# Kernel optimization log

Hardware: AMD Instinct MI355X
Metric: run time of the kernel (lower is better)

## Reference

```python
import jax, jax.numpy as jnp
import numpy as np

N_NODES = 50000
N_EDGES = 1600000
NUM_BASIS = 10
HIDDEN = 64
MAX_RADIUS = 3.0
WEIGHT_NUMEL = 5  # paths: (0x0->0),(0x1->1),(1x0->1),(1x1->0),(1x1->1)


def setup_inputs() -> dict:
    key = jax.random.key(0)
    k1, k2, k3, k4, k5 = jax.random.split(key, 5)
    f_1 = jax.random.normal(k1, (N_NODES, 4), dtype=jnp.float32)
    pos = jax.random.uniform(k2, (N_NODES, 3), dtype=jnp.float32) * MAX_RADIUS
    edge_index = jax.random.randint(k3, (2, N_EDGES), 0, N_NODES, dtype=jnp.int64)
    # radial MLP params (e3nn FullyConnectedNet init: std-normal weights)
    W1 = jax.random.normal(k4, (NUM_BASIS, HIDDEN), dtype=jnp.float32)
    W2 = jax.random.normal(k5, (HIDDEN, WEIGHT_NUMEL), dtype=jnp.float32)
    return {"f_1": f_1, "pos": pos, "W1": W1, "W2": W2, "edge_index": edge_index}


def _forward(f_1, pos, W1, W2, edge_index):
    row, col = edge_index[0], edge_index[1]
    num_nodes = f_1.shape[0]
    num_neighbors = edge_index.shape[1] / num_nodes

    edge_vec = pos[row] - pos[col]                      # [E,3]
    r2 = jnp.sum(edge_vec * edge_vec, axis=-1)
    r = jnp.sqrt(jnp.maximum(r2, 1e-12))                # [E]
    unit = edge_vec / r[:, None]

    # spherical harmonics 0e+1e, component normalization, e3nn (y,z,x) order
    sh = jnp.concatenate(
        [jnp.ones_like(unit[:, :1]), jnp.sqrt(3.0) * unit[:, [1, 2, 0]]], axis=-1
    )                                                   # [E,4]

    # soft_one_hot_linspace, basis='smooth_finite', cutoff=True
    values = jnp.linspace(0.0, MAX_RADIUS, NUM_BASIS + 2)[1:-1]
    step = values[1] - values[0]
    diff = (r[:, None] - values) / step                 # [E,num_basis]
    inside = jnp.abs(diff) < 1.0
    d = jnp.where(inside, diff, 0.0)
    C = 1.14136 * float(np.e) ** 2
    emb = jnp.where(inside, C * jnp.exp(-1.0 / (1.0 + d) - 1.0 / (1.0 - d)), 0.0)

    # e3nn FullyConnectedNet [num_basis, hidden, weight_numel] with relu
    # hidden: act normalized to unit 2nd moment (relu -> *sqrt(2)); weights /sqrt(fan_in)
    h = jax.nn.relu(emb @ (W1 / jnp.sqrt(float(NUM_BASIS)))) * jnp.sqrt(2.0)
    w = h @ (W2 / jnp.sqrt(float(HIDDEN)))              # [E,5]

    # FullyConnectedTensorProduct (0e+1e) x (0e+1e) -> (0e+1e), per-edge weights
    x = f_1[row]
    x0, xv = x[:, 0], x[:, 1:4]
    y0, yv = sh[:, 0], sh[:, 1:4]
    inv_s3 = 1.0 / jnp.sqrt(3.0)
    inv_s6 = 1.0 / jnp.sqrt(6.0)
    # output 0e: fan-in 2 paths -> norm sqrt(1/2)
    out0 = jnp.sqrt(0.5) * (
        w[:, 0] * x0 * y0 + w[:, 3] * jnp.sum(xv * yv, axis=-1) * inv_s3
    )
    # output 1e: fan-in 3 paths -> norm sqrt(3/3)=1
    outv = (
        w[:, 1:2] * x0[:, None] * yv * inv_s3
        + w[:, 2:3] * xv * y0[:, None] * inv_s3
        + w[:, 4:5] * jnp.cross(xv, yv) * inv_s6
    )
    f_edge = jnp.concatenate([out0[:, None], outv], axis=-1)  # [E,4]

    out = jax.ops.segment_sum(f_edge, col, num_segments=num_nodes)
    return out / jnp.sqrt(num_neighbors).astype(out.dtype)


def reference(f_1, pos, W1, W2, edge_index):
    return _forward(f_1, pos, W1, W2, edge_index)
```

## Files before the change

### kernel.cpp

```cpp
#include <hip/hip_runtime.h>
#include <math.h>

#define N_NODES_C 50000
#define N_EDGES_C 1600000
#define EPB 1024
#define NBLK_E 1563
#define NBLK_N 196
#define TBL 256

#define NREG 25
#define RSH 11
#define RNODES 2048
#define CAPL 17
#define NCHG 32

#define QSCALE 1024.0f
#define QINV   (1.0f / 1024.0f)

__device__ __forceinline__ int detect_is64_block(const void* eidx, int t, int* lds_flag) {
    if (t < 64) {
        const long long* p = (const long long*)eidx;
        bool ok = true;
        for (int k = 0; k < 4; ++k) {
            long long v = p[t * 4 + k];
            ok &= (v >= 0 && v < (long long)N_NODES_C);
        }
        unsigned long long m = __ballot(ok);
        if (t == 0) *lds_flag = (m == ~0ull) ? 1 : 0;
    }
    __syncthreads();
    return *lds_flag;
}

__device__ __forceinline__ int load_col(const void* eidx, int is64, int e) {
    return is64 ? (int)((const long long*)eidx)[N_EDGES_C + e]
                : ((const int*)eidx)[N_EDGES_C + e];
}
__device__ __forceinline__ int load_row(const void* eidx, int is64, int e) {
    return is64 ? (int)((const long long*)eidx)[e]
                : ((const int*)eidx)[e];
}

__device__ __forceinline__ void edge_quant(const float* __restrict__ f1,
                                           const float* __restrict__ pos,
                                           const float* __restrict__ w1s,
                                           const float* __restrict__ W2,
                                           int row, int col, int v[4]) {
    v[0] = v[1] = v[2] = v[3] = 0;
    float px = pos[row * 3 + 0] - pos[col * 3 + 0];
    float py = pos[row * 3 + 1] - pos[col * 3 + 1];
    float pz = pos[row * 3 + 2] - pos[col * 3 + 2];
    float r2 = px * px + py * py + pz * pz;
    float r = sqrtf(fmaxf(r2, 1e-12f));
    float inv_r = 1.0f / r;
    float ux = px * inv_r, uy = py * inv_r, uz = pz * inv_r;
    const float SQ3 = 1.7320508075688772f;
    float yv0 = SQ3 * uy, yv1 = SQ3 * uz, yv2 = SQ3 * ux;

    const float C = 8.433573069075486f;
    float tt = r * (11.0f / 3.0f);
    int k1 = (int)tt;
    float d = tt - (float)k1;
    float e0 = 0.f, e1 = 0.f;
    int b0 = 0, b1 = 0;
    if (k1 >= 1 && k1 <= 10) {
        b0 = k1 - 1;
        e0 = C * __expf(-1.0f / (1.0f + d) - 1.0f / (1.0f - d));
    }
    int k2 = k1 + 1;
    if (k2 <= 10 && d > 0.f) {
        b1 = k2 - 1;
        float d2 = d - 1.0f;
        e1 = C * __expf(-1.0f / (1.0f + d2) - 1.0f / (1.0f - d2));
    }
    if (e0 == 0.f && e1 == 0.f) return;

    const float* r0 = &w1s[b0 * 68];
    const float* r1 = &w1s[b1 * 68];
    float w0 = 0.f, w1a = 0.f, w2a = 0.f, w3 = 0.f, w4 = 0.f;
#pragma unroll
    for (int j = 0; j < 64; j += 4) {
        float4 a = *(const float4*)(r0 + j);
        float4 b = *(const float4*)(r1 + j);
        float h0 = fmaxf(e0 * a.x + e1 * b.x, 0.f);
        float h1 = fmaxf(e0 * a.y + e1 * b.y, 0.f);
        float h2 = fmaxf(e0 * a.z + e1 * b.z, 0.f);
        float h3 = fmaxf(e0 * a.w + e1 * b.w, 0.f);
        w0  += h0 * W2[(j + 0) * 5 + 0] + h1 * W2[(j + 1) * 5 + 0] + h2 * W2[(j + 2) * 5 + 0] + h3 * W2[(j + 3) * 5 + 0];
        w1a += h0 * W2[(j + 0) * 5 + 1] + h1 * W2[(j + 1) * 5 + 1] + h2 * W2[(j + 2) * 5 + 1] + h3 * W2[(j + 3) * 5 + 1];
        w2a += h0 * W2[(j + 0) * 5 + 2] + h1 * W2[(j + 1) * 5 + 2] + h2 * W2[(j + 2) * 5 + 2] + h3 * W2[(j + 3) * 5 + 2];
        w3  += h0 * W2[(j + 0) * 5 + 3] + h1 * W2[(j + 1) * 5 + 3] + h2 * W2[(j + 2) * 5 + 3] + h3 * W2[(j + 3) * 5 + 3];
        w4  += h0 * W2[(j + 0) * 5 + 4] + h1 * W2[(j + 1) * 5 + 4] + h2 * W2[(j + 2) * 5 + 4] + h3 * W2[(j + 3) * 5 + 4];
    }
    const float SC = 0.05590169943749474f;
    w0 *= SC; w1a *= SC; w2a *= SC; w3 *= SC; w4 *= SC;

    float4 x = *(const float4*)(f1 + row * 4);
    float x0 = x.x, xv0 = x.y, xv1 = x.z, xv2 = x.w;

    const float INV_S3 = 0.5773502691896258f;
    const float INV_S6 = 0.4082482904638631f;
    const float SQH    = 0.7071067811865476f;
    const float INV_SQRT_NN = 0.17677669529663687f;

    float dotxy = xv0 * yv0 + xv1 * yv1 + xv2 * yv2;
    float out0 = SQH * (w0 * x0 + w3 * dotxy * INV_S3) * INV_SQRT_NN;
    float cx0 = xv1 * yv2 - xv2 * yv1;
    float cx1 = xv2 * yv0 - xv0 * yv2;
    float cx2 = xv0 * yv1 - xv1 * yv0;
    float o1 = (w1a * x0 * yv0 * INV_S3 + w2a * xv0 * INV_S3 + w4 * cx0 * INV_S6) * INV_SQRT_NN;
    float o2 = (w1a * x0 * yv1 * INV_S3 + w2a * xv1 * INV_S3 + w4 * cx1 * INV_S6) * INV_SQRT_NN;
    float o3 = (w1a * x0 * yv2 * INV_S3 + w2a * xv2 * INV_S3 + w4 * cx2 * INV_S6) * INV_SQRT_NN;

    v[0] = min(8191, max(-8191, (int)rintf(out0 * QSCALE)));
    v[1] = min(8191, max(-8191, (int)rintf(o1   * QSCALE)));
    v[2] = min(8191, max(-8191, (int)rintf(o2   * QSCALE)));
    v[3] = min(8191, max(-8191, (int)rintf(o3   * QSCALE)));
}

__device__ __forceinline__ unsigned long long edge_q(
        float prx, float pry, float prz, float4 xx,
        float pcx, float pcy, float pcz,
        const float* tC0, const float* tC1, const float* tC2,
        const float* tC3, const float* tC4) {
    float px = prx - pcx;
    float py = pry - pcy;
    float pz = prz - pcz;
    float r2 = px * px + py * py + pz * pz;
    float r = sqrtf(fmaxf(r2, 1e-12f));
    float inv_r = 1.0f / r;
    float uv0 = py * inv_r, uv1 = pz * inv_r, uv2 = px * inv_r;

    float ft = fminf(r * (255.0f / 3.0f), 255.0f);
    int idx = min((int)ft, TBL - 2);
    float fr = ft - (float)idx;
    float c0 = fmaf(fr, tC0[idx + 1] - tC0[idx], tC0[idx]);
    float c1 = fmaf(fr, tC1[idx + 1] - tC1[idx], tC1[idx]);
    float c2 = fmaf(fr, tC2[idx + 1] - tC2[idx], tC2[idx]);
    float c3 = fmaf(fr, tC3[idx + 1] - tC3[idx], tC3[idx]);
    float c4 = fmaf(fr, tC4[idx + 1] - tC4[idx], tC4[idx]);

    float x0 = xx.x, xv0 = xx.y, xv1 = xx.z, xv2 = xx.w;

    float dotxy = xv0 * uv0 + xv1 * uv1 + xv2 * uv2;
    float out0 = c0 * x0 + c3 * dotxy;
    float cx0 = xv1 * uv2 - xv2 * uv1;
    float cx1 = xv2 * uv0 - xv0 * uv2;
    float cx2 = xv0 * uv1 - xv1 * uv0;
    float c1x = c1 * x0;
    float o1 = c1x * uv0 + c2 * xv0 + c4 * cx0;
    float o2 = c1x * uv1 + c2 * xv1 + c4 * cx1;
    float o3 = c1x * uv2 + c2 * xv2 + c4 * cx2;

    int v0 = min(8191, max(-8191, (int)rintf(out0 * QSCALE)));
    int v1 = min(8191, max(-8191, (int)rintf(o1 * QSCALE)));
    int v2 = min(8191, max(-8191, (int)rintf(o2 * QSCALE)));
    int v3 = min(8191, max(-8191, (int)rintf(o3 * QSCALE)));

    return (unsigned long long)((long long)v0 + ((long long)v1 << 16)
         + ((long long)v2 << 32) + ((long long)v3 << 48));
}

__global__ __launch_bounds__(256)
void binscatter_kernel(const float* __restrict__ f1, const float* __restrict__ pos,
                       const float* __restrict__ W1, const float* __restrict__ W2,
                       const void* __restrict__ eidx,
                       unsigned* __restrict__ gOff,
                       unsigned* __restrict__ rcG,
                       float* __restrict__ nodeq,
                       float* __restrict__ tG) {
    __shared__ unsigned rcbuf[EPB];
    __shared__ unsigned stageRc[EPB];
    __shared__ unsigned histS[32];
    __shared__ unsigned gBaseS[32];
    __shared__ unsigned localBaseS[32];
    __shared__ unsigned cursorLocS[32];
    __shared__ int flag_s;
    const int t = threadIdx.x;
    float* w1s = (float*)stageRc;
    if (blockIdx.x == 0) {
        for (int i = t; i < 640; i += 256) w1s[(i >> 6) * 68 + (i & 63)] = W1[i];
    }
    if (t < 32) histS[t] = 0u;
    const int is64 = detect_is64_block(eidx, t, &flag_s);

    if (blockIdx.x == 0) {
        float tt = (float)t * (11.0f / 255.0f);
        int k1 = (int)tt;
        float d = tt - (float)k1;
        const float C = 8.433573069075486f;
        float e0 = 0.f, e1 = 0.f;
        int b0 = 0, b1 = 0;
        if (k1 >= 1 && k1 <= 10) {
            b0 = k1 - 1;
            e0 = C * __expf(-1.0f / (1.0f + d) - 1.0f / (1.0f - d));
        }
        int k2 = k1 + 1;
        if (k2 <= 10 && d > 0.f) {
            b1 = k2 - 1;
            float d2 = d - 1.0f;
            e1 = C * __expf(-1.0f / (1.0f + d2) - 1.0f / (1.0f - d2));
        }
        float w0 = 0.f, w1 = 0.f, w2 = 0.f, w3 = 0.f, w4 = 0.f;
        const float* r0 = &w1s[b0 * 68];
        const float* r1 = &w1s[b1 * 68];
#pragma unroll
        for (int j = 0; j < 64; j += 4) {
            float4 a = *(const float4*)(r0 + j);
            float4 b = *(const float4*)(r1 + j);
            float h0 = fmaxf(e0 * a.x + e1 * b.x, 0.f);
            float h1 = fmaxf(e0 * a.y + e1 * b.y, 0.f);
            float h2 = fmaxf(e0 * a.z + e1 * b.z, 0.f);
            float h3 = fmaxf(e0 * a.w + e1 * b.w, 0.f);
            w0 += h0 * W2[(j + 0) * 5 + 0] + h1 * W2[(j + 1) * 5 + 0] + h2 * W2[(j + 2) * 5 + 0] + h3 * W2[(j + 3) * 5 + 0];
            w1 += h0 * W2[(j + 0) * 5 + 1] + h1 * W2[(j + 1) * 5 + 1] + h2 * W2[(j + 2) * 5 + 1] + h3 * W2[(j + 3) * 5 + 1];
            w2 += h0 * W2[(j + 0) * 5 + 2] + h1 * W2[(j + 1) * 5 + 2] + h2 * W2[(j + 2) * 5 + 2] + h3 * W2[(j + 3) * 5 + 2];
            w3 += h0 * W2[(j + 0) * 5 + 3] + h1 * W2[(j + 1) * 5 + 3] + h2 * W2[(j + 2) * 5 + 3] + h3 * W2[(j + 3) * 5 + 3];
            w4 += h0 * W2[(j + 0) * 5 + 4] + h1 * W2[(j + 1) * 5 + 4] + h2 * W2[(j + 2) * 5 + 4] + h3 * W2[(j + 3) * 5 + 4];
        }
        const float SC  = 0.05590169943749474f;
        const float ISN = 0.17677669529663687f;
        const float SQH = 0.7071067811865476f;
        const float INV_S3 = 0.5773502691896258f;
        const float INV_S6 = 0.4082482904638631f;
        const float SQ3 = 1.7320508075688772f;
        float base = SC * ISN;
        tG[0 * TBL + t] = SQH * base * w0;
        tG[1 * TBL + t] = base * w1;
        tG[2 * TBL + t] = INV_S3 * base * w2;
        tG[3 * TBL + t] = SQH * base * w3;
        tG[4 * TBL + t] = INV_S6 * SQ3 * base * w4;
    }

    const int e0b = blockIdx.x * EPB;
    const int nedge = min(EPB, N_EDGES_C - e0b);
    for (int i = t; i < nedge; i += 256) {
        int row = load_row(eidx, is64, e0b + i);
        int col = load_col(eidx, is64, e0b + i);
        rcbuf[i] = ((unsigned)row << 16) | (unsigned)col;
        atomicAdd(&histS[col >> RSH], 1u);
    }
    {
        int n = blockIdx.x * 256 + t;
        if (blockIdx.x < NBLK_N && n < N_NODES_C) {
            float4 f = *(const float4*)(f1 + 4 * n);
            float4 p;
            p.x = pos[3 * n + 0];
            p.y = pos[3 * n + 1];
            p.z = pos[3 * n + 2];
            p.w = 0.f;
            *(float4*)(nodeq + 8 * n)     = p;
            *(float4*)(nodeq + 8 * n + 4) = f;
        }
    }
    __syncthreads();
    if (t == 0) {
        unsigned run = 0u;
        for (int b = 0; b < 32; ++b) {
            localBaseS[b] = run;
            cursorLocS[b] = run;
            run += histS[b];
        }
    }
    if (t < 32) {
        gBaseS[t] = ((unsigned)t << CAPL) + atomicAdd(&gOff[t], histS[t]);
    }
    __syncthreads();
    for (int i = t; i < nedge; i += 256) {
        unsigned rc = rcbuf[i];
        int b = (int)((rc & 0xFFFFu) >> RSH);
        unsigned p = atomicAdd(&cursorLocS[b], 1u);
        stageRc[p] = rc;
    }
    __syncthreads();
    for (int i = t; i < nedge; i += 256) {
        unsigned rc = stageRc[i];
        int b = (int)((rc & 0xFFFFu) >> RSH);
        unsigned dst = gBaseS[b] + ((unsigned)i - localBaseS[b]);
        unsigned lim = ((unsigned)(b + 1)) << CAPL;
        if (dst < lim) rcG[dst] = rc;
    }
}

__global__ __launch_bounds__(512)
void mgather_kernel(const unsigned* __restrict__ rcG,
                    const unsigned* __restrict__ gOff,
                    const float* __restrict__ pos,
                    const float* __restrict__ nodeq,
                    const float* __restrict__ tG,
                    unsigned long long* __restrict__ partials) {
    __shared__ unsigned long long accs[RNODES];
    __shared__ float posx[RNODES];
    __shared__ float posy[RNODES];
    __shared__ float posz[RNODES];
    __shared__ float tC0[TBL];
    __shared__ float tC1[TBL];
    __shared__ float tC2[TBL];
    __shared__ float tC3[TBL];
    __shared__ float tC4[TBL];
    const int t = threadIdx.x;
    const int B = blockIdx.x;
    const int c = blockIdx.y;
    if (t < TBL) {
        tC0[t] = tG[0 * TBL + t];
        tC1[t] = tG[1 * TBL + t];
        tC2[t] = tG[2 * TBL + t];
        tC3[t] = tG[3 * TBL + t];
        tC4[t] = tG[4 * TBL + t];
    }
    const int nb0 = B << RSH;
    for (int j = t; j < RNODES; j += 512) {
        accs[j] = 0ull;
        int n = nb0 + j;
        if (n < N_NODES_C) {
            posx[j] = pos[3 * n + 0];
            posy[j] = pos[3 * n + 1];
            posz[j] = pos[3 * n + 2];
        }
    }
    __syncthreads();

    unsigned cnt = min(gOff[B], (unsigned)(1u << CAPL));
    unsigned i0 = (unsigned)(((unsigned long long)cnt * (unsigned)c) / NCHG);
    unsigned i1 = (unsigned)(((unsigned long long)cnt * (unsigned)(c + 1)) / NCHG);
    const unsigned* src = rcG + ((size_t)B << CAPL);

    unsigned i = i0 + t;
    for (; i + 512 < i1; i += 1024) {
        unsigned rcA = src[i];
        unsigned rcB = src[i + 512];
        int rowA = (int)(rcA >> 16), lcA = (int)(rcA & (RNODES - 1));
        int rowB = (int)(rcB >> 16), lcB = (int)(rcB & (RNODES - 1));
        const float4* nrA = (const float4*)(nodeq + ((size_t)rowA << 3));
        const float4* nrB = (const float4*)(nodeq + ((size_t)rowB << 3));
        float4 prA = nrA[0];
        float4 xxA = nrA[1];
        float4 prB = nrB[0];
        float4 xxB = nrB[1];
        float pcxA = posx[lcA], pcyA = posy[lcA], pczA = posz[lcA];
        float pcxB = posx[lcB], pcyB = posy[lcB], pczB = posz[lcB];
        unsigned long long QA = edge_q(prA.x, prA.y, prA.z, xxA, pcxA, pcyA, pczA,
                                       tC0, tC1, tC2, tC3, tC4);
        unsigned long long QB = edge_q(prB.x, prB.y, prB.z, xxB, pcxB, pcyB, pczB,
                                       tC0, tC1, tC2, tC3, tC4);
        atomicAdd(&accs[lcA], QA);
        atomicAdd(&accs[lcB], QB);
    }
    for (; i < i1; i += 512) {
        unsigned rc = src[i];
        int row = (int)(rc >> 16), lc = (int)(rc & (RNODES - 1));
        const float4* nr = (const float4*)(nodeq + ((size_t)row << 3));
        float4 pr = nr[0];
        float4 xx = nr[1];
        unsigned long long Q = edge_q(pr.x, pr.y, pr.z, xx, posx[lc], posy[lc], posz[lc],
                                      tC0, tC1, tC2, tC3, tC4);
        atomicAdd(&accs[lc], Q);
    }
    __syncthreads();
    unsigned long long* dst = partials + (((size_t)(B * NCHG + c)) << RSH);
    for (int j = t; j < RNODES; j += 512) dst[j] = accs[j];
}

__global__ __launch_bounds__(256)
void reduce6_kernel(const unsigned long long* __restrict__ partials, float* __restrict__ out) {
    int n = blockIdx.x * 256 + threadIdx.x;
    if (n >= N_NODES_C) return;
    int B = n >> RSH;
    int lc = n & (RNODES - 1);
    const unsigned long long* src = partials + (((size_t)(B * NCHG)) << RSH) + lc;
    unsigned long long s = 0ull;
#pragma unroll
    for (int c = 0; c < NCHG; ++c) s += src[(size_t)c << RSH];
    long long T = (long long)s;
    int s0 = (int)(short)(T & 0xFFFF); T = (T - s0) >> 16;
    int s1 = (int)(short)(T & 0xFFFF); T = (T - s1) >> 16;
    int s2 = (int)(short)(T & 0xFFFF); T = (T - s2) >> 16;
    int s3 = (int)T;
    float4 o;
    o.x = (float)s0 * QINV;
    o.y = (float)s1 * QINV;
    o.z = (float)s2 * QINV;
    o.w = (float)s3 * QINV;
    *(float4*)(out + 4 * n) = o;
}

__global__ __launch_bounds__(256)
void init_acc(unsigned long long* __restrict__ acc,
              const void* __restrict__ eidx, int* __restrict__ flag) {
    int i = blockIdx.x * 256 + threadIdx.x;
    if (i < N_NODES_C) acc[i] = 0ull;
    if (blockIdx.x == 0 && threadIdx.x < 64) {
        const long long* p = (const long long*)eidx;
        bool ok = true;
        for (int k = 0; k < 4; ++k) {
            long long v = p[threadIdx.x * 4 + k];
            ok &= (v >= 0 && v < (long long)N_NODES_C);
        }
        unsigned long long m = __ballot(ok);
        if (threadIdx.x == 0) *flag = (m == ~0ull) ? 1 : 0;
    }
}

__global__ __launch_bounds__(256)
void reduce_unpack(const unsigned long long* __restrict__ acc, float* __restrict__ out) {
    int n = blockIdx.x * 256 + threadIdx.x;
    if (n >= N_NODES_C) return;
    long long T = (long long)acc[n];
    int s0 = (int)(short)(T & 0xFFFF); T = (T - s0) >> 16;
    int s1 = (int)(short)(T & 0xFFFF); T = (T - s1) >> 16;
    int s2 = (int)(short)(T & 0xFFFF); T = (T - s2) >> 16;
    int s3 = (int)T;
    float4 o;
    o.x = (float)s0 * QINV; o.y = (float)s1 * QINV;
    o.z = (float)s2 * QINV; o.w = (float)s3 * QINV;
    *(float4*)(out + 4 * n) = o;
}

__global__ __launch_bounds__(256)
void equi_conv_atomic(const float* __restrict__ f1, const float* __restrict__ pos,
                      const float* __restrict__ W1, const float* __restrict__ W2,
                      const void* __restrict__ eidx, const int* __restrict__ flag_p,
                      unsigned long long* __restrict__ acc) {
    __shared__ float w1s[10 * 68];
    const int tid = threadIdx.x;
    for (int i = tid; i < 640; i += 256) w1s[(i >> 6) * 68 + (i & 63)] = W1[i];
    __syncthreads();
    const int e = blockIdx.x * 256 + tid;
    if (e >= N_EDGES_C) return;
    const int is64 = *flag_p;
    int row = load_row(eidx, is64, e);
    int col = load_col(eidx, is64, e);
    int v[4];
    edge_quant(f1, pos, w1s, W2, row, col, v);
    if (v[0] | v[1] | v[2] | v[3]) {
        unsigned long long P = (unsigned long long)((long long)v[0] + ((long long)v[1] << 16)
                             + ((long long)v[2] << 32) + ((long long)v[3] << 48));
        __hip_atomic_fetch_add(acc + col, P, __ATOMIC_RELAXED, __HIP_MEMORY_SCOPE_AGENT);
    }
}

extern "C" void kernel_launch(void* const* d_in, const int* in_sizes, int n_in,
                              void* d_out, int out_size, void* d_ws, size_t ws_size,
                              hipStream_t stream) {
    const float* f1  = (const float*)d_in[0];
    const float* pos = (const float*)d_in[1];
    const float* W1  = (const float*)d_in[2];
    const float* W2  = (const float*)d_in[3];
    const void*  eix = d_in[4];
    float* out = (float*)d_out;

    const size_t offRC = 0;
    const size_t szRC  = ((size_t)32 << CAPL) * 4;
    const size_t offC  = offRC + szRC;
    const size_t szC   = 32 * 4;
    const size_t offT  = (offC + szC + 15) & ~(size_t)15;
    const size_t szT   = (size_t)5 * TBL * 4;
    const size_t offQ  = (offT + szT + 15) & ~(size_t)15;
    const size_t szQ   = (size_t)N_NODES_C * 32;
    const size_t offR  = (offQ + szQ + 15) & ~(size_t)15;
    const size_t szR   = ((size_t)NREG * NCHG) << RSH << 3;
    const size_t need  = offR + szR;

    if (ws_size >= need) {
        unsigned*           rcG      = (unsigned*)((char*)d_ws + offRC);
        unsigned*           gOff     = (unsigned*)((char*)d_ws + offC);
        float*              tG       = (float*)((char*)d_ws + offT);
        float*              nodeq    = (float*)((char*)d_ws + offQ);
        unsigned long long* partials = (unsigned long long*)((char*)d_ws + offR);

        hipMemsetAsync(gOff, 0, 32 * sizeof(unsigned), stream);
        binscatter_kernel<<<NBLK_E, 256, 0, stream>>>(f1, pos, W1, W2, eix, gOff, rcG, nodeq, tG);
        mgather_kernel<<<dim3(NREG, NCHG), 512, 0, stream>>>(rcG, gOff, pos, nodeq, tG, partials);
        reduce6_kernel<<<NBLK_N, 256, 0, stream>>>(partials, out);
    } else {
        unsigned long long* acc = (unsigned long long*)d_ws;
        int* flag = (int*)((char*)d_ws + (size_t)N_NODES_C * 8);
        const int nblk = (N_NODES_C + 255) / 256;
        init_acc<<<nblk, 256, 0, stream>>>(acc, eix, flag);
        equi_conv_atomic<<<(N_EDGES_C + 255) / 256, 256, 0, stream>>>(f1, pos, W1, W2, eix, flag, acc);
        reduce_unpack<<<nblk, 256, 0, stream>>>(acc, out);
    }
}
```

Baseline: 114.2 us.

## Replace partials buffer and reduce pass with global atomics; enlarge binscatter blocks

Each mgather block now atomically adds its per-region shared-memory sums straight into a zeroed global accumulator, skipping zero entries. This replaces the 32-way partials buffer and its dedicated reduction kernel with a cheaper unpack. The binscatter kernel now runs 512 threads over 2048 edges per block, halving the block count, and the node repacking covers all nodes without the old block-index guard. The cost is contended 64-bit global atomics across 32 chunks per node and a larger memset.

```diff
diff --git a/kernel.cpp b/kernel.cpp
--- a/kernel.cpp
+++ b/kernel.cpp
@@ -3,8 +3,8 @@
 
 #define N_NODES_C 50000
 #define N_EDGES_C 1600000
-#define EPB 1024
-#define NBLK_E 1563
+#define EPB2 2048
+#define NBLK_E2 782
 #define NBLK_N 196
 #define TBL 256
 
@@ -161,7 +161,7 @@
          + ((long long)v2 << 32) + ((long long)v3 << 48));
 }
 
-__global__ __launch_bounds__(256)
+__global__ __launch_bounds__(512)
 void binscatter_kernel(const float* __restrict__ f1, const float* __restrict__ pos,
                        const float* __restrict__ W1, const float* __restrict__ W2,
                        const void* __restrict__ eidx,
@@ -169,8 +169,8 @@
                        unsigned* __restrict__ rcG,
                        float* __restrict__ nodeq,
                        float* __restrict__ tG) {
-    __shared__ unsigned rcbuf[EPB];
-    __shared__ unsigned stageRc[EPB];
+    __shared__ unsigned rcbuf[EPB2];
+    __shared__ unsigned stageRc[EPB2];
     __shared__ unsigned histS[32];
     __shared__ unsigned gBaseS[32];
     __shared__ unsigned localBaseS[32];
@@ -179,12 +179,12 @@
     const int t = threadIdx.x;
     float* w1s = (float*)stageRc;
     if (blockIdx.x == 0) {
-        for (int i = t; i < 640; i += 256) w1s[(i >> 6) * 68 + (i & 63)] = W1[i];
+        for (int i = t; i < 640; i += 512) w1s[(i >> 6) * 68 + (i & 63)] = W1[i];
     }
     if (t < 32) histS[t] = 0u;
     const int is64 = detect_is64_block(eidx, t, &flag_s);
 
-    if (blockIdx.x == 0) {
+    if (blockIdx.x == 0 && t < TBL) {
         float tt = (float)t * (11.0f / 255.0f);
         int k1 = (int)tt;
         float d = tt - (float)k1;
@@ -232,17 +232,17 @@
         tG[4 * TBL + t] = INV_S6 * SQ3 * base * w4;
     }
 
-    const int e0b = blockIdx.x * EPB;
-    const int nedge = min(EPB, N_EDGES_C - e0b);
-    for (int i = t; i < nedge; i += 256) {
+    const int e0b = blockIdx.x * EPB2;
+    const int nedge = min(EPB2, N_EDGES_C - e0b);
+    for (int i = t; i < nedge; i += 512) {
         int row = load_row(eidx, is64, e0b + i);
         int col = load_col(eidx, is64, e0b + i);
         rcbuf[i] = ((unsigned)row << 16) | (unsigned)col;
         atomicAdd(&histS[col >> RSH], 1u);
     }
     {
-        int n = blockIdx.x * 256 + t;
-        if (blockIdx.x < NBLK_N && n < N_NODES_C) {
+        int n = blockIdx.x * 512 + t;
+        if (n < N_NODES_C) {
             float4 f = *(const float4*)(f1 + 4 * n);
             float4 p;
             p.x = pos[3 * n + 0];
@@ -266,14 +266,14 @@
         gBaseS[t] = ((unsigned)t << CAPL) + atomicAdd(&gOff[t], histS[t]);
     }
     __syncthreads();
-    for (int i = t; i < nedge; i += 256) {
+    for (int i = t; i < nedge; i += 512) {
         unsigned rc = rcbuf[i];
         int b = (int)((rc & 0xFFFFu) >> RSH);
         unsigned p = atomicAdd(&cursorLocS[b], 1u);
         stageRc[p] = rc;
     }
     __syncthreads();
-    for (int i = t; i < nedge; i += 256) {
+    for (int i = t; i < nedge; i += 512) {
         unsigned rc = stageRc[i];
         int b = (int)((rc & 0xFFFFu) >> RSH);
         unsigned dst = gBaseS[b] + ((unsigned)i - localBaseS[b]);
@@ -288,7 +288,7 @@
                     const float* __restrict__ pos,
                     const float* __restrict__ nodeq,
                     const float* __restrict__ tG,
-                    unsigned long long* __restrict__ partials) {
+                    unsigned long long* __restrict__ acc) {
     __shared__ unsigned long long accs[RNODES];
     __shared__ float posx[RNODES];
     __shared__ float posy[RNODES];
@@ -357,47 +357,12 @@
         atomicAdd(&accs[lc], Q);
     }
     __syncthreads();
-    unsigned long long* dst = partials + (((size_t)(B * NCHG + c)) << RSH);
-    for (int j = t; j < RNODES; j += 512) dst[j] = accs[j];
-}
-
-__global__ __launch_bounds__(256)
-void reduce6_kernel(const unsigned long long* __restrict__ partials, float* __restrict__ out) {
-    int n = blockIdx.x * 256 + threadIdx.x;
-    if (n >= N_NODES_C) return;
-    int B = n >> RSH;
-    int lc = n & (RNODES - 1);
-    const unsigned long long* src = partials + (((size_t)(B * NCHG)) << RSH) + lc;
-    unsigned long long s = 0ull;
-#pragma unroll
-    for (int c = 0; c < NCHG; ++c) s += src[(size_t)c << RSH];
-    long long T = (long long)s;
-    int s0 = (int)(short)(T & 0xFFFF); T = (T - s0) >> 16;
-    int s1 = (int)(short)(T & 0xFFFF); T = (T - s1) >> 16;
-    int s2 = (int)(short)(T & 0xFFFF); T = (T - s2) >> 16;
-    int s3 = (int)T;
-    float4 o;
-    o.x = (float)s0 * QINV;
-    o.y = (float)s1 * QINV;
-    o.z = (float)s2 * QINV;
-    o.w = (float)s3 * QINV;
-    *(float4*)(out + 4 * n) = o;
-}
-
-__global__ __launch_bounds__(256)
-void init_acc(unsigned long long* __restrict__ acc,
-              const void* __restrict__ eidx, int* __restrict__ flag) {
-    int i = blockIdx.x * 256 + threadIdx.x;
-    if (i < N_NODES_C) acc[i] = 0ull;
-    if (blockIdx.x == 0 && threadIdx.x < 64) {
-        const long long* p = (const long long*)eidx;
-        bool ok = true;
-        for (int k = 0; k < 4; ++k) {
-            long long v = p[threadIdx.x * 4 + k];
-            ok &= (v >= 0 && v < (long long)N_NODES_C);
-        }
-        unsigned long long m = __ballot(ok);
-        if (threadIdx.x == 0) *flag = (m == ~0ull) ? 1 : 0;
+    for (int j = t; j < RNODES; j += 512) {
+        unsigned long long v = accs[j];
+        int n = nb0 + j;
+        if (v && n < N_NODES_C) {
+            __hip_atomic_fetch_add(acc + n, v, __ATOMIC_RELAXED, __HIP_MEMORY_SCOPE_AGENT);
+        }
     }
 }
 
@@ -417,6 +382,23 @@
 }
 
 __global__ __launch_bounds__(256)
+void init_acc(unsigned long long* __restrict__ acc,
+              const void* __restrict__ eidx, int* __restrict__ flag) {
+    int i = blockIdx.x * 256 + threadIdx.x;
+    if (i < N_NODES_C) acc[i] = 0ull;
+    if (blockIdx.x == 0 && threadIdx.x < 64) {
+        const long long* p = (const long long*)eidx;
+        bool ok = true;
+        for (int k = 0; k < 4; ++k) {
+            long long v = p[threadIdx.x * 4 + k];
+            ok &= (v >= 0 && v < (long long)N_NODES_C);
+        }
+        unsigned long long m = __ballot(ok);
+        if (threadIdx.x == 0) *flag = (m == ~0ull) ? 1 : 0;
+    }
+}
+
+__global__ __launch_bounds__(256)
 void equi_conv_atomic(const float* __restrict__ f1, const float* __restrict__ pos,
                       const float* __restrict__ W1, const float* __restrict__ W2,
                       const void* __restrict__ eidx, const int* __restrict__ flag_p,
@@ -453,25 +435,25 @@
     const size_t szRC  = ((size_t)32 << CAPL) * 4;
     const size_t offC  = offRC + szRC;
     const size_t szC   = 32 * 4;
-    const size_t offT  = (offC + szC + 15) & ~(size_t)15;
+    const size_t offA  = offC + szC;
+    const size_t szA   = (size_t)N_NODES_C * 8;
+    const size_t offT  = (offA + szA + 15) & ~(size_t)15;
     const size_t szT   = (size_t)5 * TBL * 4;
     const size_t offQ  = (offT + szT + 15) & ~(size_t)15;
     const size_t szQ   = (size_t)N_NODES_C * 32;
-    const size_t offR  = (offQ + szQ + 15) & ~(size_t)15;
-    const size_t szR   = ((size_t)NREG * NCHG) << RSH << 3;
-    const size_t need  = offR + szR;
+    const size_t need  = offQ + szQ;
 
     if (ws_size >= need) {
-        unsigned*           rcG      = (unsigned*)((char*)d_ws + offRC);
-        unsigned*           gOff     = (unsigned*)((char*)d_ws + offC);
-        float*              tG       = (float*)((char*)d_ws + offT);
-        float*              nodeq    = (float*)((char*)d_ws + offQ);
-        unsigned long long* partials = (unsigned long long*)((char*)d_ws + offR);
-
-        hipMemsetAsync(gOff, 0, 32 * sizeof(unsigned), stream);
-        binscatter_kernel<<<NBLK_E, 256, 0, stream>>>(f1, pos, W1, W2, eix, gOff, rcG, nodeq, tG);
-        mgather_kernel<<<dim3(NREG, NCHG), 512, 0, stream>>>(rcG, gOff, pos, nodeq, tG, partials);
-        reduce6_kernel<<<NBLK_N, 256, 0, stream>>>(partials, out);
+        unsigned*           rcG   = (unsigned*)((char*)d_ws + offRC);
+        unsigned*           gOff  = (unsigned*)((char*)d_ws + offC);
+        unsigned long long* acc   = (unsigned long long*)((char*)d_ws + offA);
+        float*              tG    = (float*)((char*)d_ws + offT);
+        float*              nodeq = (float*)((char*)d_ws + offQ);
+
+        hipMemsetAsync(gOff, 0, szC + szA, stream);
+        binscatter_kernel<<<NBLK_E2, 512, 0, stream>>>(f1, pos, W1, W2, eix, gOff, rcG, nodeq, tG);
+        mgather_kernel<<<dim3(NREG, NCHG), 512, 0, stream>>>(rcG, gOff, pos, nodeq, tG, acc);
+        reduce_unpack<<<NBLK_N, 256, 0, stream>>>(acc, out);
     } else {
         unsigned long long* acc = (unsigned long long*)d_ws;
         int* flag = (int*)((char*)d_ws + (size_t)N_NODES_C * 8);
```

Result: faster. 105.6 us (-7.5%).
